# Kernel optimization log

Hardware: AMD Instinct MI355X
Metric: run time of the kernel (lower is better)

Reference implementation:

```python
import jax, jax.numpy as jnp
import numpy as np

B, H, S, DK, DV = 2, 16, 2048, 64, 64

def setup_inputs() -> dict:
    key = jax.random.key(0)
    kq, kk, kv, km = jax.random.split(key, 4)
    q = jax.random.normal(kq, (B, H, S, DK), dtype=jnp.float32)
    k = jax.random.normal(kk, (B, H, S, DK), dtype=jnp.float32)
    v = jax.random.normal(kv, (B, H, S, DV), dtype=jnp.float32)
    mask = jax.random.randint(km, (B, H, S, S), 0, 2).astype(jnp.bool_)
    return {"q": q, "k": k, "v": v, "mask": mask}

def reference(q, k, v, mask):
    d_k = q.shape[-1]
    # scores: [B, H, Sq, Sk]
    scores = jnp.einsum('bhqd,bhkd->bhqk', q, k) / np.sqrt(d_k).astype(jnp.float32)
    scores = jnp.where(mask, jnp.float32(-1e9), scores)
    attn = jax.nn.softmax(scores, axis=-1)
    return jnp.einsum('bhqk,bhkd->bhqd', attn, v)
```

## Files before the change

kernel.cpp:

```cpp
#include <hip/hip_runtime.h>


#define LOG2E 1.4426950408889634f
#define QSCALE (0.125f * LOG2E)

typedef __attribute__((ext_vector_type(8))) short short8;
typedef __attribute__((ext_vector_type(4))) short short4v;
typedef __attribute__((ext_vector_type(4))) float f32x4;
typedef unsigned __attribute__((ext_vector_type(4))) uintv4;

constexpr int S = 2048, D = 64;

__device__ __forceinline__ short bf16rne(float x) {
  union { float f; unsigned u; } cv; cv.f = x;
  unsigned u = cv.u;
  u += 0x7fffu + ((u >> 16) & 1u);
  return (short)(u >> 16);
}

__device__ __forceinline__ void glds16(const void* g, void* l) {
  __builtin_amdgcn_global_load_lds(
      (const __attribute__((address_space(1))) void*)g,
      (__attribute__((address_space(3))) void*)l, 16, 0, 0);
}

__global__ void prep(const float* __restrict__ kp, const float* __restrict__ vp,
                     short* __restrict__ kb, short* __restrict__ vt,
                     const unsigned* __restrict__ m, int* __restrict__ flag) {
  const int b = blockIdx.x;
  const int tid = threadIdx.x;
  if (b == 0 && tid < 64) {
    unsigned v = m[tid];
    unsigned long long big = __ballot(v > 1u && v != 0x3F800000u);
    unsigned long long isf = __ballot(v == 0x3F800000u);
    if (tid == 0) *flag = (big != 0ull && isf == 0ull) ? 1 : 0;
  }
  if (b < 2048) {
    size_t i = ((size_t)b * 256 + tid) * 8;
    float4 a = *(const float4*)(kp + i);
    float4 c = *(const float4*)(kp + i + 4);
    short8 s;
    s[0] = bf16rne(a.x); s[1] = bf16rne(a.y); s[2] = bf16rne(a.z); s[3] = bf16rne(a.w);
    s[4] = bf16rne(c.x); s[5] = bf16rne(c.y); s[6] = bf16rne(c.z); s[7] = bf16rne(c.w);
    *(short8*)&kb[i] = s;
  } else {
    __shared__ float tile[64][65];
    const int bb = b - 2048;
    const int bh = bb >> 5, k0 = (bb & 31) * 64;
    const float* src = vp + ((size_t)(bh * S + k0)) * D;
#pragma unroll
    for (int i = 0; i < 4; ++i) {
      int row = i * 16 + (tid >> 4);
      int col = (tid & 15) * 4;
      float4 x = *(const float4*)(src + row * D + col);
      tile[row][col] = x.x; tile[row][col + 1] = x.y;
      tile[row][col + 2] = x.z; tile[row][col + 3] = x.w;
    }
    __syncthreads();
#pragma unroll
    for (int i = 0; i < 4; ++i) {
      int dim = i * 16 + (tid >> 4);
      int kb4 = (tid & 15) * 4;
      short4v s;
#pragma unroll
      for (int j = 0; j < 4; ++j) s[j] = bf16rne(tile[kb4 + j][dim]);
      *(short4v*)&vt[((size_t)(bh * D + dim)) * S + k0 + kb4] = s;
    }
  }
}

__launch_bounds__(256, 4)
__global__ void attn_fwd(const float* __restrict__ qp, const short* __restrict__ kb,
                         const short* __restrict__ vt, const void* __restrict__ mp,
                         float* __restrict__ op, const int* __restrict__ fmtp) {
  const int fmt  = *fmtp;
  const int tid  = threadIdx.x;
  const int lane = tid & 63;
  const int w    = tid >> 6;
  const int c    = lane & 15;
  const int quad = lane >> 4;
  const int kh   = w & 1;
  const int qh   = w >> 1;

  const int bid = (blockIdx.x & 7) * 128 + (blockIdx.x >> 3);
  const int bh  = bid >> 5;
  const int q0  = (bid & 31) * 64;

  __shared__ __align__(16) char smem[32768];
  short* ksb = (short*)smem;
  short* vsb = (short*)(smem + 16384);
  float* Osc = (float*)smem;
  float* Lsc = (float*)(smem + 17000);

  short8 qB[2][2];
#pragma unroll
  for (int qg = 0; qg < 2; ++qg) {
    const float* qg_p = qp + ((size_t)(bh * S + q0 + qh * 32 + qg * 16 + c)) * D;
#pragma unroll
    for (int kk = 0; kk < 2; ++kk) {
      const float* p = qg_p + kk * 32 + quad * 8;
      float4 x = *(const float4*)(p);
      float4 y = *(const float4*)(p + 4);
      short8 f;
      f[0] = bf16rne(x.x * QSCALE); f[1] = bf16rne(x.y * QSCALE);
      f[2] = bf16rne(x.z * QSCALE); f[3] = bf16rne(x.w * QSCALE);
      f[4] = bf16rne(y.x * QSCALE); f[5] = bf16rne(y.y * QSCALE);
      f[6] = bf16rne(y.z * QSCALE); f[7] = bf16rne(y.w * QSCALE);
      qB[qg][kk] = f;
    }
  }

  f32x4 O[2][4];
#pragma unroll
  for (int qg = 0; qg < 2; ++qg)
#pragma unroll
    for (int dt = 0; dt < 4; ++dt) O[qg][dt] = (f32x4){0.f, 0.f, 0.f, 0.f};
  float Lp[2] = {0.f, 0.f};

  const int rsub = lane >> 3;
  const int csw  = (lane & 7) ^ rsub;
  const short* kbase = kb + ((size_t)(bh * S)) * D;
  const short* vbase = vt + ((size_t)(bh * D)) * S;

  const size_t mro0 = ((size_t)(bh * S + q0 + qh * 32 + c)) * S;
  const size_t mro1 = mro0 + (size_t)16 * S;

  unsigned long long mm[2];

  auto stage = [&](int it, int buf) {
    const int k0 = it * 64;
#pragma unroll
    for (int h2 = 0; h2 < 2; ++h2) {
      const int row = (h2 * 4 + w) * 8 + rsub;
      glds16(kbase + (size_t)(k0 + row) * 64 + csw * 8,
             (char*)&ksb[buf * 4096] + (h2 * 4 + w) * 1024);
      glds16(vbase + (size_t)row * S + k0 + csw * 8,
             (char*)&vsb[buf * 4096] + (h2 * 4 + w) * 1024);
    }
  };

  auto mload = [&](int it) {
    const int kO = it * 64 + kh * 32;
    if (fmt == 1) {
#pragma unroll
      for (int qg = 0; qg < 2; ++qg)
        mm[qg] = __builtin_nontemporal_load((const unsigned long long*)
            ((const unsigned char*)mp + (qg ? mro1 : mro0) + kO + 8 * quad));
    } else {
#pragma unroll
      for (int qg = 0; qg < 2; ++qg) {
        const unsigned* m0 = (const unsigned*)mp + (qg ? mro1 : mro0) + kO + 8 * quad;
        uintv4 a = __builtin_nontemporal_load((const uintv4*)m0);
        uintv4 b = __builtin_nontemporal_load((const uintv4*)(m0 + 4));
        unsigned long long t = 0ull;
#pragma unroll
        for (int j = 0; j < 4; ++j) {
          if (a[j]) t |= 0xffull << (8 * j);
          if (b[j]) t |= 0xffull << (8 * (j + 4));
        }
        mm[qg] = t;
      }
    }
  };

  stage(0, 0);
  mload(0);

  for (int it = 0; it < 32; ++it) {
    const int buf = it & 1;
    __syncthreads();

    if (it + 1 < 32) stage(it + 1, buf ^ 1);

    unsigned long long mb0 = mm[0], mb1 = mm[1];
    if (it + 1 < 32) mload(it + 1);

    short8 ka[2][2];
#pragma unroll
    for (int kt = 0; kt < 2; ++kt) {
      const int rr = kh * 32 + 8 * (c >> 2) + (c & 3) + 4 * kt;
      const int r7 = (c & 3) + 4 * kt;
#pragma unroll
      for (int kk = 0; kk < 2; ++kk)
        ka[kt][kk] =
            *(const short8*)&ksb[buf * 4096 + rr * 64 + (((kk * 4 + quad) ^ r7) * 8)];
    }
    short8 vb[4];
#pragma unroll
    for (int dt = 0; dt < 4; ++dt)
      vb[dt] = *(const short8*)&vsb[buf * 4096 + (dt * 16 + c) * 64 +
                                    (((kh * 4 + quad) ^ (c & 7)) * 8)];

#pragma unroll
    for (int qg = 0; qg < 2; ++qg) {
      f32x4 z0 = (f32x4){0.f, 0.f, 0.f, 0.f};
      f32x4 z1 = (f32x4){0.f, 0.f, 0.f, 0.f};
      z0 = __builtin_amdgcn_mfma_f32_16x16x32_bf16(ka[0][0], qB[qg][0], z0, 0, 0, 0);
      z0 = __builtin_amdgcn_mfma_f32_16x16x32_bf16(ka[0][1], qB[qg][1], z0, 0, 0, 0);
      z1 = __builtin_amdgcn_mfma_f32_16x16x32_bf16(ka[1][0], qB[qg][0], z1, 0, 0, 0);
      z1 = __builtin_amdgcn_mfma_f32_16x16x32_bf16(ka[1][1], qB[qg][1], z1, 0, 0, 0);

      short8 pf;
      float part = 0.f;
      const unsigned long long mq = qg ? mb1 : mb0;
#pragma unroll
      for (int j = 0; j < 8; ++j) {
        float zv = (j < 4) ? z0[j & 3] : z1[j & 3];
        float e = ((mq >> (8 * j)) & 0xffull) ? 0.f : exp2f(zv);
        part += e;
        pf[j] = bf16rne(e);
      }
      Lp[qg] += part;

#pragma unroll
      for (int dt = 0; dt < 4; ++dt)
        O[qg][dt] =
            __builtin_amdgcn_mfma_f32_16x16x32_bf16(pf, vb[dt], O[qg][dt], 0, 0, 0);
    }
  }

  float Lq[2];
#pragma unroll
  for (int qg = 0; qg < 2; ++qg) {
    float t = Lp[qg];
    t += __shfl_xor(t, 16);
    t += __shfl_xor(t, 32);
    Lq[qg] = t;
  }

  __syncthreads();
  if (kh == 1) {
#pragma unroll
    for (int qg = 0; qg < 2; ++qg) {
#pragma unroll
      for (int dt = 0; dt < 4; ++dt)
#pragma unroll
        for (int r = 0; r < 4; ++r)
          Osc[(qh * 32 + qg * 16 + quad * 4 + r) * 66 + dt * 16 + c] = O[qg][dt][r];
    }
    if (quad == 0) {
      Lsc[qh * 32 + c]      = Lq[0];
      Lsc[qh * 32 + 16 + c] = Lq[1];
    }
  }
  __syncthreads();
  if (kh == 0) {
#pragma unroll
    for (int qg = 0; qg < 2; ++qg)
#pragma unroll
      for (int r = 0; r < 4; ++r) {
        const int qrow = qg * 16 + quad * 4 + r;
        float Ls = __shfl(Lq[qg], (lane & 48) | (quad * 4 + r)) + Lsc[qh * 32 + qrow];
        float inv = 1.f / Ls;
        const size_t ob = ((size_t)(bh * S + q0 + qh * 32 + qrow)) * D;
#pragma unroll
        for (int dt = 0; dt < 4; ++dt)
          op[ob + dt * 16 + c] =
              (O[qg][dt][r] + Osc[(qh * 32 + qrow) * 66 + dt * 16 + c]) * inv;
      }
  }
}

extern "C" void kernel_launch(void* const* d_in, const int* in_sizes, int n_in,
                              void* d_out, int out_size, void* d_ws, size_t ws_size,
                              hipStream_t stream) {
  const float* q = (const float*)d_in[0];
  const float* k = (const float*)d_in[1];
  const float* v = (const float*)d_in[2];
  const void*  m = d_in[3];

  short* kbuf = (short*)d_ws;
  short* vtb  = (short*)((char*)d_ws + (8u << 20));
  int* flag   = (int*)((char*)d_ws + (16u << 20));

  prep<<<3072, 256, 0, stream>>>(k, v, kbuf, vtb, (const unsigned*)m, flag);
  attn_fwd<<<1024, 256, 0, stream>>>(q, kbuf, vtb, m, (float*)d_out, flag);
}
```

Baseline: 787.3 us.

## Remove block swizzle, add extra K-tile LDS swizzle, and reorder MFMA loop by key tile

Drops the XCD-interleaving block-index remap and uses blockIdx directly for (bh, q0). Adds an extra XOR term to the K tile's LDS layout based on wave parity and the lane's row group, presumably to reduce LDS bank conflicts on K fragment reads. Restructures the inner loop to iterate over key tiles, computing both query groups per loaded K fragment, and loads each V fragment just before its MFMA pair. This is meant to lower register pressure and improve interleaving, at the risk of changing L2 locality across XCDs.

```diff
diff --git a/kernel.cpp b/kernel.cpp
--- a/kernel.cpp
+++ b/kernel.cpp
@@ -82,9 +82,8 @@
   const int kh   = w & 1;
   const int qh   = w >> 1;
 
-  const int bid = (blockIdx.x & 7) * 128 + (blockIdx.x >> 3);
-  const int bh  = bid >> 5;
-  const int q0  = (bid & 31) * 64;
+  const int bh = blockIdx.x >> 5;
+  const int q0 = (blockIdx.x & 31) * 64;
 
   __shared__ __align__(16) char smem[32768];
   short* ksb = (short*)smem;
@@ -118,10 +117,13 @@
   float Lp[2] = {0.f, 0.f};
 
   const int rsub = lane >> 3;
-  const int csw  = (lane & 7) ^ rsub;
+  const int cswV = (lane & 7) ^ rsub;
+  const int cswK = cswV ^ ((w & 1) << 2);
   const short* kbase = kb + ((size_t)(bh * S)) * D;
   const short* vbase = vt + ((size_t)(bh * D)) * S;
 
+  const int kx = (((c >> 2) & 1) << 2);
+
   const size_t mro0 = ((size_t)(bh * S + q0 + qh * 32 + c)) * S;
   const size_t mro1 = mro0 + (size_t)16 * S;
 
@@ -132,9 +134,9 @@
 #pragma unroll
     for (int h2 = 0; h2 < 2; ++h2) {
       const int row = (h2 * 4 + w) * 8 + rsub;
-      glds16(kbase + (size_t)(k0 + row) * 64 + csw * 8,
+      glds16(kbase + (size_t)(k0 + row) * 64 + cswK * 8,
              (char*)&ksb[buf * 4096] + (h2 * 4 + w) * 1024);
-      glds16(vbase + (size_t)row * S + k0 + csw * 8,
+      glds16(vbase + (size_t)row * S + k0 + cswV * 8,
              (char*)&vsb[buf * 4096] + (h2 * 4 + w) * 1024);
     }
   };
@@ -172,50 +174,41 @@
 
     if (it + 1 < 32) stage(it + 1, buf ^ 1);
 
-    unsigned long long mb0 = mm[0], mb1 = mm[1];
+    const unsigned long long mb0 = mm[0], mb1 = mm[1];
     if (it + 1 < 32) mload(it + 1);
 
-    short8 ka[2][2];
+    short8 pf0, pf1;
+    float part0 = 0.f, part1 = 0.f;
 #pragma unroll
     for (int kt = 0; kt < 2; ++kt) {
-      const int rr = kh * 32 + 8 * (c >> 2) + (c & 3) + 4 * kt;
       const int r7 = (c & 3) + 4 * kt;
-#pragma unroll
-      for (int kk = 0; kk < 2; ++kk)
-        ka[kt][kk] =
-            *(const short8*)&ksb[buf * 4096 + rr * 64 + (((kk * 4 + quad) ^ r7) * 8)];
-    }
-    short8 vb[4];
-#pragma unroll
-    for (int dt = 0; dt < 4; ++dt)
-      vb[dt] = *(const short8*)&vsb[buf * 4096 + (dt * 16 + c) * 64 +
-                                    (((kh * 4 + quad) ^ (c & 7)) * 8)];
-
-#pragma unroll
-    for (int qg = 0; qg < 2; ++qg) {
+      const int rr = kh * 32 + 8 * (c >> 2) + r7;
+      const int px = (quad ^ r7 ^ kx) * 8;
+      short8 ka0 = *(const short8*)&ksb[buf * 4096 + rr * 64 + px];
+      short8 ka1 = *(const short8*)&ksb[buf * 4096 + rr * 64 + (px ^ 32)];
       f32x4 z0 = (f32x4){0.f, 0.f, 0.f, 0.f};
       f32x4 z1 = (f32x4){0.f, 0.f, 0.f, 0.f};
-      z0 = __builtin_amdgcn_mfma_f32_16x16x32_bf16(ka[0][0], qB[qg][0], z0, 0, 0, 0);
-      z0 = __builtin_amdgcn_mfma_f32_16x16x32_bf16(ka[0][1], qB[qg][1], z0, 0, 0, 0);
-      z1 = __builtin_amdgcn_mfma_f32_16x16x32_bf16(ka[1][0], qB[qg][0], z1, 0, 0, 0);
-      z1 = __builtin_amdgcn_mfma_f32_16x16x32_bf16(ka[1][1], qB[qg][1], z1, 0, 0, 0);
-
-      short8 pf;
-      float part = 0.f;
-      const unsigned long long mq = qg ? mb1 : mb0;
-#pragma unroll
-      for (int j = 0; j < 8; ++j) {
-        float zv = (j < 4) ? z0[j & 3] : z1[j & 3];
-        float e = ((mq >> (8 * j)) & 0xffull) ? 0.f : exp2f(zv);
-        part += e;
-        pf[j] = bf16rne(e);
+      z0 = __builtin_amdgcn_mfma_f32_16x16x32_bf16(ka0, qB[0][0], z0, 0, 0, 0);
+      z0 = __builtin_amdgcn_mfma_f32_16x16x32_bf16(ka1, qB[0][1], z0, 0, 0, 0);
+      z1 = __builtin_amdgcn_mfma_f32_16x16x32_bf16(ka0, qB[1][0], z1, 0, 0, 0);
+      z1 = __builtin_amdgcn_mfma_f32_16x16x32_bf16(ka1, qB[1][1], z1, 0, 0, 0);
+#pragma unroll
+      for (int r = 0; r < 4; ++r) {
+        const int j = 4 * kt + r;
+        float e0 = ((mb0 >> (8 * j)) & 0xffull) ? 0.f : exp2f(z0[r]);
+        float e1 = ((mb1 >> (8 * j)) & 0xffull) ? 0.f : exp2f(z1[r]);
+        part0 += e0; part1 += e1;
+        pf0[j] = bf16rne(e0); pf1[j] = bf16rne(e1);
       }
-      Lp[qg] += part;
-
-#pragma unroll
-      for (int dt = 0; dt < 4; ++dt)
-        O[qg][dt] =
-            __builtin_amdgcn_mfma_f32_16x16x32_bf16(pf, vb[dt], O[qg][dt], 0, 0, 0);
+    }
+    Lp[0] += part0; Lp[1] += part1;
+
+#pragma unroll
+    for (int dt = 0; dt < 4; ++dt) {
+      short8 vb = *(const short8*)&vsb[buf * 4096 + (dt * 16 + c) * 64 +
+                                       (((kh * 4 + quad) ^ (c & 7)) * 8)];
+      O[0][dt] = __builtin_amdgcn_mfma_f32_16x16x32_bf16(pf0, vb, O[0][dt], 0, 0, 0);
+      O[1][dt] = __builtin_amdgcn_mfma_f32_16x16x32_bf16(pf1, vb, O[1][dt], 0, 0, 0);
     }
   }
 
```

Result: no change. 776.3 us (-1.4%).
